# Kernel optimization log

Measured on AMD Instinct MI355X. Metric: run time of the kernel, lower is better.

The kernel has to match this reference:

```python
import jax, jax.numpy as jnp
import numpy as np

LN_EPS = 1e-12


def setup_inputs() -> dict:
    key = jax.random.key(0)
    ks = jax.random.split(key, 10)
    B, S, W, D, H = 16, 512, 5, 200, 768
    std = 0.02
    return {
        "layer_output": jax.random.normal(ks[0], (B, S, H), dtype=jnp.float32),
        "word_embeddings": jax.random.normal(ks[1], (B, S, W, D), dtype=jnp.float32),
        "word_mask": jax.random.randint(ks[2], (B, S, W), 0, 2, dtype=jnp.int64),
        "W1": jax.random.normal(ks[3], (D, H), dtype=jnp.float32) * std,
        "b1": jnp.zeros((H,), dtype=jnp.float32),
        "W2": jax.random.normal(ks[4], (H, H), dtype=jnp.float32) * std,
        "b2": jnp.zeros((H,), dtype=jnp.float32),
        "attn_W": jax.random.normal(ks[5], (H, H), dtype=jnp.float32) * std,
        "ln_gamma": jnp.ones((H,), dtype=jnp.float32),
        "ln_beta": jnp.zeros((H,), dtype=jnp.float32),
    }


def reference(layer_output, word_embeddings, word_mask, W1, b1, W2, b2, attn_W, ln_gamma, ln_beta):
    # word_transform: Linear -> Tanh -> Linear (dropout = identity in eval)
    we = jnp.tanh(jnp.einsum("bswd,dh->bswh", word_embeddings, W1) + b1)
    we = jnp.einsum("bswh,hk->bswk", we, W2) + b2  # [B,S,W,H]

    # bilinear word attention: (x @ attn_W) . word_outputs -> score over W
    q = jnp.einsum("bsh,hk->bsk", layer_output, attn_W)  # [B,S,H]
    alpha = jnp.einsum("bsk,bswk->bsw", q, we)            # [B,S,W]
    alpha = alpha + (1.0 - word_mask.astype(alpha.dtype)) * -10000.0
    alpha = jax.nn.softmax(alpha, axis=-1)

    # weighted sum over words + residual
    agg = jnp.einsum("bsw,bswh->bsh", alpha, we)
    h = layer_output + agg

    # LayerNorm (fuse_layer; dropout = identity in eval)
    mu = jnp.mean(h, axis=-1, keepdims=True)
    var = jnp.mean(jnp.square(h - mu), axis=-1, keepdims=True)
    return (h - mu) * jax.lax.rsqrt(var + LN_EPS) * ln_gamma + ln_beta
```

## Files before the change

kernel.cpp:

```cpp
#include <hip/hip_runtime.h>
#include <hip/hip_bf16.h>
#include <math.h>


typedef __attribute__((ext_vector_type(8))) short bf16x8;
typedef __attribute__((ext_vector_type(4))) float f32x4;

__device__ __forceinline__ unsigned short f2bf_bits(float f) {
    __hip_bfloat16 h = __float2bfloat16(f);
    return *reinterpret_cast<unsigned short*>(&h);
}
__device__ __forceinline__ float bf_bits2f(unsigned short u) {
    union { unsigned int i; float f; } v; v.i = ((unsigned int)u) << 16; return v.f;
}
__device__ __forceinline__ float tanh_fast(float x) {
    float xc = fminf(fmaxf(x, -9.f), 9.f);
    float t  = __expf(2.f * xc);
    return (t - 1.f) * __builtin_amdgcn_rcpf(t + 1.f);
}

__device__ __forceinline__ void async_cp16(const void* g, void* lds) {
#if __has_builtin(__builtin_amdgcn_global_load_lds)
    auto gp = (const __attribute__((address_space(1))) unsigned int*)g;
    auto lp = (__attribute__((address_space(3))) unsigned int*)lds;
    __builtin_amdgcn_global_load_lds(gp, lp, 16, 0, 0);
#else
    *(uint4*)lds = *(const uint4*)g;
#endif
}

template<bool HAS_BIAS, bool TANH_ACT, bool RESID, bool OUT_BF16, int N, int K, int GX>
__global__ __launch_bounds__(256) void mfma_gemm(
    const __hip_bfloat16* __restrict__ A,
    const __hip_bfloat16* __restrict__ Bt,
    const float* __restrict__ bias,
    const float* __restrict__ resid,
    void* __restrict__ outp)
{
    __shared__ __align__(16) unsigned char smem[32768];
    unsigned short* As = (unsigned short*)smem;
    unsigned short* Bs = (unsigned short*)(smem + 16384);

    int bx, by;
    {
        const int total = gridDim.x;
        const int per_xcd = total >> 3;
        if ((total & 7) == 0 && (per_xcd % GX) == 0) {
            int xcd = blockIdx.x & 7, idx = blockIdx.x >> 3;
            int lin = xcd * per_xcd + idx;
            by = lin / GX; bx = lin % GX;
        } else { by = blockIdx.x / GX; bx = blockIdx.x % GX; }
    }
    const int m0 = by * 128;
    const int n0 = bx * 128;

    const int tid  = threadIdx.x;
    const int lane = tid & 63;
    const int wave = tid >> 6;
    const int wm   = wave & 1;
    const int wn   = wave >> 1;

    const int rsub = lane >> 3;
    const int slot = lane & 7;
    const int kc   = slot ^ rsub;
    const __hip_bfloat16* gA = A  + (size_t)(m0 + wave * 32 + rsub) * K + kc * 8;
    const __hip_bfloat16* gB = Bt + (size_t)(n0 + wave * 32 + rsub) * K + kc * 8;
    unsigned short* lA = As + wave * 2048 + lane * 8;
    unsigned short* lB = Bs + wave * 2048 + lane * 8;

    const int row16 = lane & 15;
    const int kq    = lane >> 4;

    f32x4 acc[4][4];
#pragma unroll
    for (int i = 0; i < 4; i++)
#pragma unroll
        for (int j = 0; j < 4; j++) acc[i][j] = (f32x4){0.f, 0.f, 0.f, 0.f};

    for (int k0 = 0; k0 < K; k0 += 64) {
#pragma unroll
        for (int i = 0; i < 4; i++) {
            async_cp16(gA + i * 8 * K, lA + i * 512);
            async_cp16(gB + i * 8 * K, lB + i * 512);
        }
        gA += 64; gB += 64;
        __syncthreads();

        bf16x8 af[2][4], bg[2][4];
#pragma unroll
        for (int kh = 0; kh < 2; kh++) {
#pragma unroll
            for (int mi = 0; mi < 4; mi++) {
                const int r = wm * 64 + mi * 16 + row16;
                const int s = (kh * 4 + kq) ^ (r & 7);
                af[kh][mi] = *(const bf16x8*)&As[r * 64 + s * 8];
            }
#pragma unroll
            for (int ni = 0; ni < 4; ni++) {
                const int r = wn * 64 + ni * 16 + row16;
                const int s = (kh * 4 + kq) ^ (r & 7);
                bg[kh][ni] = *(const bf16x8*)&Bs[r * 64 + s * 8];
            }
        }
#pragma unroll
        for (int kh = 0; kh < 2; kh++)
#pragma unroll
            for (int mi = 0; mi < 4; mi++)
#pragma unroll
                for (int ni = 0; ni < 4; ni++)
                    acc[mi][ni] = __builtin_amdgcn_mfma_f32_16x16x32_bf16(
                        af[kh][mi], bg[kh][ni], acc[mi][ni], 0, 0, 0);
        __syncthreads();
    }

    if (OUT_BF16) {
        unsigned short* rep = (unsigned short*)smem;
#pragma unroll
        for (int ni = 0; ni < 4; ni++) {
            const int c = wn * 64 + ni * 16 + row16;
            float bcol = HAS_BIAS ? bias[n0 + c] : 0.f;
#pragma unroll
            for (int mi = 0; mi < 4; mi++)
#pragma unroll
                for (int r = 0; r < 4; r++) {
                    const int rr = wm * 64 + mi * 16 + kq * 4 + r;
                    float v = acc[mi][ni][r];
                    if (HAS_BIAS) v += bcol;
                    if (TANH_ACT) v = tanh_fast(v);
                    rep[rr * 128 + c] = f2bf_bits(v);
                }
        }
        __syncthreads();
#pragma unroll
        for (int p = 0; p < 8; p++) {
            const int lin = p * 256 + tid;
            const int row = lin >> 4;
            const int c8  = lin & 15;
            uint4 d = *(const uint4*)&rep[row * 128 + c8 * 8];
            *(uint4*)((__hip_bfloat16*)outp + (size_t)(m0 + row) * N + n0 + c8 * 8) = d;
        }
    } else {
        float* rep = (float*)smem;
#pragma unroll
        for (int h = 0; h < 2; h++) {
            if (wm == h) {
#pragma unroll
                for (int ni = 0; ni < 4; ni++) {
                    const int c = wn * 64 + ni * 16 + row16;
                    float bcol = HAS_BIAS ? bias[n0 + c] : 0.f;
#pragma unroll
                    for (int mi = 0; mi < 4; mi++)
#pragma unroll
                        for (int r = 0; r < 4; r++) {
                            const int rr = mi * 16 + kq * 4 + r;
                            float v = acc[mi][ni][r];
                            if (HAS_BIAS) v += bcol;
                            if (TANH_ACT) v = tanh_fast(v);
                            rep[rr * 128 + c] = v;
                        }
                }
            }
            __syncthreads();
#pragma unroll
            for (int p = 0; p < 8; p++) {
                const int lin = p * 256 + tid;
                const int row = lin >> 5;
                const int c4  = lin & 31;
                float4 v = *(const float4*)&rep[row * 128 + c4 * 4];
                const int grow = m0 + h * 64 + row;
                if (RESID) {
                    float4 rv = *(const float4*)&resid[(size_t)grow * N + n0 + c4 * 4];
                    v.x += rv.x; v.y += rv.y; v.z += rv.z; v.w += rv.w;
                }
                *(float4*)((float*)outp + (size_t)grow * N + n0 + c4 * 4) = v;
            }
            __syncthreads();
        }
    }
}

__global__ __launch_bounds__(256) void prep_kernel(
    const float* __restrict__ x,  __hip_bfloat16* __restrict__ xb,
    const float* __restrict__ w2, __hip_bfloat16* __restrict__ w2b,
    const float* __restrict__ aw, __hip_bfloat16* __restrict__ awb,
    const float* __restrict__ E,  __hip_bfloat16* __restrict__ Eb,
    const float* __restrict__ W1, __hip_bfloat16* __restrict__ W1Tb,
    __hip_bfloat16* __restrict__ W2Tb)
{
    __shared__ float tile[32][33];
    const int b = blockIdx.x, tid = threadIdx.x;
    if (b < 6144 + 576 + 576) {
        const float* src; __hip_bfloat16* dst; long long i;
        if (b < 6144)      { src = x;  dst = xb;  i = (long long)b * 256 + tid; }
        else if (b < 6720) { src = w2; dst = w2b; i = (long long)(b - 6144) * 256 + tid; }
        else               { src = aw; dst = awb; i = (long long)(b - 6720) * 256 + tid; }
        float4 v = ((const float4*)src)[i];
        ((ushort4*)dst)[i] = make_ushort4(f2bf_bits(v.x), f2bf_bits(v.y), f2bf_bits(v.z), f2bf_bits(v.w));
    } else if (b < 7296 + 10240) {
        const int lane = tid & 63, wave = tid >> 6;
        const long long row = (long long)(b - 7296) * 4 + wave;
        const int k = lane * 4;
        float4 v = make_float4(0.f, 0.f, 0.f, 0.f);
        if (k < 200) v = *(const float4*)&E[row * 200 + k];
        *(ushort4*)&Eb[row * 256 + k] =
            make_ushort4(f2bf_bits(v.x), f2bf_bits(v.y), f2bf_bits(v.z), f2bf_bits(v.w));
    } else {
        const float* in; __hip_bfloat16* outb; int R, C, Rpad, t;
        if (b < 17536 + 192) { t = b - 17536; in = W1; outb = W1Tb; R = 200; C = 768; Rpad = 256; }
        else                 { t = b - 17728; in = w2; outb = W2Tb; R = 768; C = 768; Rpad = 768; }
        const int c0 = (t % 24) * 32, r0 = (t / 24) * 32;
        const int xx = tid & 31, yy = tid >> 5;
#pragma unroll
        for (int i = 0; i < 32; i += 8) {
            int r = r0 + yy + i;
            tile[yy + i][xx] = (r < R) ? in[(size_t)r * C + c0 + xx] : 0.f;
        }
        __syncthreads();
#pragma unroll
        for (int i = 0; i < 32; i += 8)
            outb[(size_t)(c0 + yy + i) * Rpad + r0 + xx] = __float2bfloat16(tile[xx][yy + i]);
    }
}

__global__ __launch_bounds__(256) void attn_kernel(
    const __hip_bfloat16* __restrict__ T,
    const __hip_bfloat16* P,
    const int* __restrict__ mask,
    __hip_bfloat16* S)
{
    const int lane = threadIdx.x & 63;
    const int wave = threadIdx.x >> 6;
    const int r    = blockIdx.x * 4 + wave;
    const int base = lane * 12;

    float pv[12];
    {
        const ushort4* pp = (const ushort4*)((const unsigned short*)P + (size_t)r * 768 + base);
        ushort4 u0 = pp[0], u1 = pp[1], u2 = pp[2];
        unsigned short us[12] = {u0.x,u0.y,u0.z,u0.w, u1.x,u1.y,u1.z,u1.w, u2.x,u2.y,u2.z,u2.w};
#pragma unroll
        for (int j = 0; j < 12; j++) pv[j] = bf_bits2f(us[j]);
    }
    float tv[5][12], part[5];
#pragma unroll
    for (int w = 0; w < 5; w++) {
        const ushort4* tp = (const ushort4*)((const unsigned short*)T + ((size_t)r * 5 + w) * 768 + base);
        ushort4 u0 = tp[0], u1 = tp[1], u2 = tp[2];
        unsigned short us[12] = {u0.x,u0.y,u0.z,u0.w, u1.x,u1.y,u1.z,u1.w, u2.x,u2.y,u2.z,u2.w};
        float s = 0.f;
#pragma unroll
        for (int j = 0; j < 12; j++) { tv[w][j] = bf_bits2f(us[j]); s += tv[w][j] * pv[j]; }
        part[w] = s;
    }
#pragma unroll
    for (int off = 32; off > 0; off >>= 1)
#pragma unroll
        for (int w = 0; w < 5; w++)
            part[w] += __shfl_xor(part[w], off, 64);

    float logit[5], mx = -1e30f;
#pragma unroll
    for (int w = 0; w < 5; w++) {
        float m = (float)mask[(size_t)r * 5 + w];
        logit[w] = part[w] - 10000.0f * (1.0f - m);
        mx = fmaxf(mx, logit[w]);
    }
    float se = 0.f;
#pragma unroll
    for (int w = 0; w < 5; w++) { logit[w] = expf(logit[w] - mx); se += logit[w]; }
    const float inv = 1.0f / se;

    unsigned short os[12];
#pragma unroll
    for (int j = 0; j < 12; j++) {
        float s = 0.f;
#pragma unroll
        for (int w = 0; w < 5; w++) s += logit[w] * tv[w][j];
        os[j] = f2bf_bits(s * inv);
    }
    ushort4* sp = (ushort4*)((unsigned short*)S + (size_t)r * 768 + base);
    sp[0] = make_ushort4(os[0], os[1], os[2],  os[3]);
    sp[1] = make_ushort4(os[4], os[5], os[6],  os[7]);
    sp[2] = make_ushort4(os[8], os[9], os[10], os[11]);
}

__global__ __launch_bounds__(256) void ln_kernel(
    const float* __restrict__ Hbuf, const float* __restrict__ gamma,
    const float* __restrict__ beta, float* __restrict__ out)
{
    const int lane = threadIdx.x & 63;
    const int wave = threadIdx.x >> 6;
    const int r    = blockIdx.x * 4 + wave;
    const float* hr = Hbuf + (size_t)r * 768 + lane * 12;

    float v[12];
    {
        float4 a = *(const float4*)(hr);
        float4 b = *(const float4*)(hr + 4);
        float4 c = *(const float4*)(hr + 8);
        v[0]=a.x; v[1]=a.y; v[2]=a.z; v[3]=a.w;
        v[4]=b.x; v[5]=b.y; v[6]=b.z; v[7]=b.w;
        v[8]=c.x; v[9]=c.y; v[10]=c.z; v[11]=c.w;
    }
    float s = 0.f;
#pragma unroll
    for (int j = 0; j < 12; j++) s += v[j];
#pragma unroll
    for (int off = 32; off > 0; off >>= 1) s += __shfl_xor(s, off, 64);
    const float mu = s * (1.f / 768.f);
    float vs = 0.f;
#pragma unroll
    for (int j = 0; j < 12; j++) { float d = v[j] - mu; vs += d * d; }
#pragma unroll
    for (int off = 32; off > 0; off >>= 1) vs += __shfl_xor(vs, off, 64);
    const float rs = rsqrtf(vs * (1.f / 768.f) + 1e-12f);

    float o[12];
#pragma unroll
    for (int j = 0; j < 12; j++) {
        int h = lane * 12 + j;
        o[j] = (v[j] - mu) * rs * gamma[h] + beta[h];
    }
    float* orow = out + (size_t)r * 768 + lane * 12;
    *(float4*)(orow)     = make_float4(o[0], o[1], o[2],  o[3]);
    *(float4*)(orow + 4) = make_float4(o[4], o[5], o[6],  o[7]);
    *(float4*)(orow + 8) = make_float4(o[8], o[9], o[10], o[11]);
}

extern "C" void kernel_launch(void* const* d_in, const int* in_sizes, int n_in,
                              void* d_out, int out_size, void* d_ws, size_t ws_size,
                              hipStream_t stream)
{
    const float* x      = (const float*)d_in[0];
    const float* E      = (const float*)d_in[1];
    const int*   mask   = (const int*)d_in[2];
    const float* W1     = (const float*)d_in[3];
    const float* b1     = (const float*)d_in[4];
    const float* W2     = (const float*)d_in[5];
    const float* b2     = (const float*)d_in[6];
    const float* attn_W = (const float*)d_in[7];
    const float* gamma  = (const float*)d_in[8];
    const float* beta   = (const float*)d_in[9];
    float* out = (float*)d_out;

    const int BS = 8192, H = 768, M1 = 40960, KP = 256;

    char* p = (char*)d_ws;
    auto alloc = [&](size_t bytes) { char* q = p; p += (bytes + 255) & ~(size_t)255; return q; };
    __hip_bfloat16* xb    = (__hip_bfloat16*)alloc((size_t)BS * H * 2);
    __hip_bfloat16* W2b   = (__hip_bfloat16*)alloc((size_t)H * H * 2);
    __hip_bfloat16* W2Tb  = (__hip_bfloat16*)alloc((size_t)H * H * 2);
    __hip_bfloat16* attnb = (__hip_bfloat16*)alloc((size_t)H * H * 2);
    __hip_bfloat16* Ctb   = (__hip_bfloat16*)alloc((size_t)H * H * 2);
    __hip_bfloat16* W1Tb  = (__hip_bfloat16*)alloc((size_t)H * KP * 2);
    __hip_bfloat16* Tb    = (__hip_bfloat16*)alloc((size_t)M1 * H * 2);
    __hip_bfloat16* Eb    = (__hip_bfloat16*)alloc((size_t)M1 * KP * 2);
    float* Hb = (float*)Tb;
    __hip_bfloat16* Pb = Eb;
    __hip_bfloat16* Sb = Pb;

    prep_kernel<<<18304, 256, 0, stream>>>(x, xb, W2, W2b, attn_W, attnb,
                                           E, Eb, W1, W1Tb, W2Tb);

    mfma_gemm<false, false, false, true, 768, 768, 6><<<36, 256, 0, stream>>>(
        W2b, attnb, nullptr, nullptr, Ctb);
    mfma_gemm<true, true, false, true, 768, 256, 6><<<1920, 256, 0, stream>>>(
        Eb, W1Tb, b1, nullptr, Tb);
    mfma_gemm<false, false, false, true, 768, 768, 6><<<384, 256, 0, stream>>>(
        xb, Ctb, nullptr, nullptr, Pb);
    attn_kernel<<<BS / 4, 256, 0, stream>>>(Tb, Pb, mask, Sb);
    mfma_gemm<true, false, true, false, 768, 768, 6><<<384, 256, 0, stream>>>(
        Sb, W2Tb, b2, x, Hb);
    ln_kernel<<<BS / 4, 256, 0, stream>>>(Hb, gamma, beta, out);
}
```

Before: 234.0 us.

## Fuse fp32-to-bf16 conversion of inputs into GEMM tile loads

Removes the separate prep pass that converted x, W2, attn_W and the word embeddings to bf16 (with K padding to 256), and instead has the GEMM load fp32 directly, convert in registers and store bf16 into LDS, zero-masking K beyond 200. This avoids writing and re-reading large bf16 intermediate buffers, notably the 40960x256 embedding copy. The trade-off is that these loads become synchronous register loads instead of async global-to-LDS copies, which may reduce latency hiding inside the GEMM main loop.

```diff
diff --git a/kernel.cpp b/kernel.cpp
--- a/kernel.cpp
+++ b/kernel.cpp
@@ -29,10 +29,20 @@
 #endif
 }
 
-template<bool HAS_BIAS, bool TANH_ACT, bool RESID, bool OUT_BF16, int N, int K, int GX>
+__device__ __forceinline__ void cvt8_store(const float* src, bool valid, unsigned short* lds) {
+    float4 v0 = make_float4(0.f, 0.f, 0.f, 0.f), v1 = v0;
+    if (valid) { v0 = *(const float4*)src; v1 = *(const float4*)(src + 4); }
+    alignas(16) unsigned short h[8] = {
+        f2bf_bits(v0.x), f2bf_bits(v0.y), f2bf_bits(v0.z), f2bf_bits(v0.w),
+        f2bf_bits(v1.x), f2bf_bits(v1.y), f2bf_bits(v1.z), f2bf_bits(v1.w)};
+    *(uint4*)lds = *(const uint4*)h;
+}
+
+template<bool HAS_BIAS, bool TANH_ACT, bool RESID, bool OUT_BF16,
+         bool A_F32, bool B_F32, int N, int K, int KASRC, int GX>
 __global__ __launch_bounds__(256) void mfma_gemm(
-    const __hip_bfloat16* __restrict__ A,
-    const __hip_bfloat16* __restrict__ Bt,
+    const void* __restrict__ A,
+    const void* __restrict__ Bt,
     const float* __restrict__ bias,
     const float* __restrict__ resid,
     void* __restrict__ outp)
@@ -63,8 +73,11 @@
     const int rsub = lane >> 3;
     const int slot = lane & 7;
     const int kc   = slot ^ rsub;
-    const __hip_bfloat16* gA = A  + (size_t)(m0 + wave * 32 + rsub) * K + kc * 8;
-    const __hip_bfloat16* gB = Bt + (size_t)(n0 + wave * 32 + rsub) * K + kc * 8;
+
+    const __hip_bfloat16* gA = (const __hip_bfloat16*)A  + (size_t)(m0 + wave * 32 + rsub) * K + kc * 8;
+    const __hip_bfloat16* gB = (const __hip_bfloat16*)Bt + (size_t)(n0 + wave * 32 + rsub) * K + kc * 8;
+    const float* gAf = (const float*)A  + (size_t)(m0 + wave * 32 + rsub) * KASRC + kc * 8;
+    const float* gBf = (const float*)Bt + (size_t)(n0 + wave * 32 + rsub) * K + kc * 8;
     unsigned short* lA = As + wave * 2048 + lane * 8;
     unsigned short* lB = Bs + wave * 2048 + lane * 8;
 
@@ -78,12 +91,15 @@
         for (int j = 0; j < 4; j++) acc[i][j] = (f32x4){0.f, 0.f, 0.f, 0.f};
 
     for (int k0 = 0; k0 < K; k0 += 64) {
+        const bool avalid = !A_F32 || (k0 + kc * 8 < KASRC);
 #pragma unroll
         for (int i = 0; i < 4; i++) {
-            async_cp16(gA + i * 8 * K, lA + i * 512);
-            async_cp16(gB + i * 8 * K, lB + i * 512);
-        }
-        gA += 64; gB += 64;
+            if (A_F32) cvt8_store(gAf + (size_t)(8 * i) * KASRC, avalid, lA + i * 512);
+            else       async_cp16(gA + (size_t)(8 * i) * K, lA + i * 512);
+            if (B_F32) cvt8_store(gBf + (size_t)(8 * i) * K, true, lB + i * 512);
+            else       async_cp16(gB + (size_t)(8 * i) * K, lB + i * 512);
+        }
+        gA += 64; gB += 64; gAf += 64; gBf += 64;
         __syncthreads();
 
         bf16x8 af[2][4], bg[2][4];
@@ -180,46 +196,25 @@
 }
 
 __global__ __launch_bounds__(256) void prep_kernel(
-    const float* __restrict__ x,  __hip_bfloat16* __restrict__ xb,
-    const float* __restrict__ w2, __hip_bfloat16* __restrict__ w2b,
-    const float* __restrict__ aw, __hip_bfloat16* __restrict__ awb,
-    const float* __restrict__ E,  __hip_bfloat16* __restrict__ Eb,
     const float* __restrict__ W1, __hip_bfloat16* __restrict__ W1Tb,
-    __hip_bfloat16* __restrict__ W2Tb)
+    const float* __restrict__ W2, __hip_bfloat16* __restrict__ W2Tb)
 {
     __shared__ float tile[32][33];
     const int b = blockIdx.x, tid = threadIdx.x;
-    if (b < 6144 + 576 + 576) {
-        const float* src; __hip_bfloat16* dst; long long i;
-        if (b < 6144)      { src = x;  dst = xb;  i = (long long)b * 256 + tid; }
-        else if (b < 6720) { src = w2; dst = w2b; i = (long long)(b - 6144) * 256 + tid; }
-        else               { src = aw; dst = awb; i = (long long)(b - 6720) * 256 + tid; }
-        float4 v = ((const float4*)src)[i];
-        ((ushort4*)dst)[i] = make_ushort4(f2bf_bits(v.x), f2bf_bits(v.y), f2bf_bits(v.z), f2bf_bits(v.w));
-    } else if (b < 7296 + 10240) {
-        const int lane = tid & 63, wave = tid >> 6;
-        const long long row = (long long)(b - 7296) * 4 + wave;
-        const int k = lane * 4;
-        float4 v = make_float4(0.f, 0.f, 0.f, 0.f);
-        if (k < 200) v = *(const float4*)&E[row * 200 + k];
-        *(ushort4*)&Eb[row * 256 + k] =
-            make_ushort4(f2bf_bits(v.x), f2bf_bits(v.y), f2bf_bits(v.z), f2bf_bits(v.w));
-    } else {
-        const float* in; __hip_bfloat16* outb; int R, C, Rpad, t;
-        if (b < 17536 + 192) { t = b - 17536; in = W1; outb = W1Tb; R = 200; C = 768; Rpad = 256; }
-        else                 { t = b - 17728; in = w2; outb = W2Tb; R = 768; C = 768; Rpad = 768; }
-        const int c0 = (t % 24) * 32, r0 = (t / 24) * 32;
-        const int xx = tid & 31, yy = tid >> 5;
-#pragma unroll
-        for (int i = 0; i < 32; i += 8) {
-            int r = r0 + yy + i;
-            tile[yy + i][xx] = (r < R) ? in[(size_t)r * C + c0 + xx] : 0.f;
-        }
-        __syncthreads();
-#pragma unroll
-        for (int i = 0; i < 32; i += 8)
-            outb[(size_t)(c0 + yy + i) * Rpad + r0 + xx] = __float2bfloat16(tile[xx][yy + i]);
-    }
+    const float* in; __hip_bfloat16* outb; int R, C, Rpad, t;
+    if (b < 192) { t = b;       in = W1; outb = W1Tb; R = 200; C = 768; Rpad = 256; }
+    else         { t = b - 192; in = W2; outb = W2Tb; R = 768; C = 768; Rpad = 768; }
+    const int c0 = (t % 24) * 32, r0 = (t / 24) * 32;
+    const int xx = tid & 31, yy = tid >> 5;
+#pragma unroll
+    for (int i = 0; i < 32; i += 8) {
+        int r = r0 + yy + i;
+        tile[yy + i][xx] = (r < R) ? in[(size_t)r * C + c0 + xx] : 0.f;
+    }
+    __syncthreads();
+#pragma unroll
+    for (int i = 0; i < 32; i += 8)
+        outb[(size_t)(c0 + yy + i) * Rpad + r0 + xx] = __float2bfloat16(tile[xx][yy + i]);
 }
 
 __global__ __launch_bounds__(256) void attn_kernel(
@@ -347,29 +342,24 @@
 
     char* p = (char*)d_ws;
     auto alloc = [&](size_t bytes) { char* q = p; p += (bytes + 255) & ~(size_t)255; return q; };
-    __hip_bfloat16* xb    = (__hip_bfloat16*)alloc((size_t)BS * H * 2);
-    __hip_bfloat16* W2b   = (__hip_bfloat16*)alloc((size_t)H * H * 2);
     __hip_bfloat16* W2Tb  = (__hip_bfloat16*)alloc((size_t)H * H * 2);
-    __hip_bfloat16* attnb = (__hip_bfloat16*)alloc((size_t)H * H * 2);
     __hip_bfloat16* Ctb   = (__hip_bfloat16*)alloc((size_t)H * H * 2);
     __hip_bfloat16* W1Tb  = (__hip_bfloat16*)alloc((size_t)H * KP * 2);
     __hip_bfloat16* Tb    = (__hip_bfloat16*)alloc((size_t)M1 * H * 2);
-    __hip_bfloat16* Eb    = (__hip_bfloat16*)alloc((size_t)M1 * KP * 2);
+    __hip_bfloat16* Pb    = (__hip_bfloat16*)alloc((size_t)BS * H * 2);
     float* Hb = (float*)Tb;
-    __hip_bfloat16* Pb = Eb;
     __hip_bfloat16* Sb = Pb;
 
-    prep_kernel<<<18304, 256, 0, stream>>>(x, xb, W2, W2b, attn_W, attnb,
-                                           E, Eb, W1, W1Tb, W2Tb);
-
-    mfma_gemm<false, false, false, true, 768, 768, 6><<<36, 256, 0, stream>>>(
-        W2b, attnb, nullptr, nullptr, Ctb);
-    mfma_gemm<true, true, false, true, 768, 256, 6><<<1920, 256, 0, stream>>>(
-        Eb, W1Tb, b1, nullptr, Tb);
-    mfma_gemm<false, false, false, true, 768, 768, 6><<<384, 256, 0, stream>>>(
-        xb, Ctb, nullptr, nullptr, Pb);
+    prep_kernel<<<768, 256, 0, stream>>>(W1, W1Tb, W2, W2Tb);
+
+    mfma_gemm<false, false, false, true, true, true, 768, 768, 768, 6>
+        <<<36, 256, 0, stream>>>(W2, attn_W, nullptr, nullptr, Ctb);
+    mfma_gemm<true, true, false, true, true, false, 768, 256, 200, 6>
+        <<<1920, 256, 0, stream>>>(E, W1Tb, b1, nullptr, Tb);
+    mfma_gemm<false, false, false, true, true, false, 768, 768, 768, 6>
+        <<<384, 256, 0, stream>>>(x, Ctb, nullptr, nullptr, Pb);
     attn_kernel<<<BS / 4, 256, 0, stream>>>(Tb, Pb, mask, Sb);
-    mfma_gemm<true, false, true, false, 768, 768, 6><<<384, 256, 0, stream>>>(
-        Sb, W2Tb, b2, x, Hb);
+    mfma_gemm<true, false, true, false, false, false, 768, 768, 768, 6>
+        <<<384, 256, 0, stream>>>(Sb, W2Tb, b2, x, Hb);
     ln_kernel<<<BS / 4, 256, 0, stream>>>(Hb, gamma, beta, out);
 }
```

Result: slower. 251.4 us (+7.4%).

## Merge small Ct GEMM into first-layer GEMM launch and skip padded K tail

Applied to the files above, without the earlier changes.

Moves the GEMM body into a device function and launches the W2·attn_W product (36 tiles) and the E·W1 tanh GEMM (1920 tiles) together in one kernel. This removes a tiny, poorly occupied launch and the serialization between them. It also adds a KREAL template parameter so the padded last K half-step of the K=256 (real 200) GEMM skips its LDS reads and MFMAs. The K loop is now fully unrolled, which may raise register pressure or code size.

```diff
diff --git a/kernel.cpp b/kernel.cpp
--- a/kernel.cpp
+++ b/kernel.cpp
@@ -29,30 +29,17 @@
 #endif
 }
 
-template<bool HAS_BIAS, bool TANH_ACT, bool RESID, bool OUT_BF16, int N, int K, int GX>
-__global__ __launch_bounds__(256) void mfma_gemm(
+template<bool HAS_BIAS, bool TANH_ACT, bool RESID, bool OUT_BF16, int N, int K, int KREAL>
+__device__ __forceinline__ void gemm_body(
     const __hip_bfloat16* __restrict__ A,
     const __hip_bfloat16* __restrict__ Bt,
     const float* __restrict__ bias,
     const float* __restrict__ resid,
-    void* __restrict__ outp)
-{
-    __shared__ __align__(16) unsigned char smem[32768];
+    void* __restrict__ outp,
+    int m0, int n0, unsigned char* smem)
+{
     unsigned short* As = (unsigned short*)smem;
     unsigned short* Bs = (unsigned short*)(smem + 16384);
-
-    int bx, by;
-    {
-        const int total = gridDim.x;
-        const int per_xcd = total >> 3;
-        if ((total & 7) == 0 && (per_xcd % GX) == 0) {
-            int xcd = blockIdx.x & 7, idx = blockIdx.x >> 3;
-            int lin = xcd * per_xcd + idx;
-            by = lin / GX; bx = lin % GX;
-        } else { by = blockIdx.x / GX; bx = blockIdx.x % GX; }
-    }
-    const int m0 = by * 128;
-    const int n0 = bx * 128;
 
     const int tid  = threadIdx.x;
     const int lane = tid & 63;
@@ -77,39 +64,45 @@
 #pragma unroll
         for (int j = 0; j < 4; j++) acc[i][j] = (f32x4){0.f, 0.f, 0.f, 0.f};
 
+#pragma unroll
     for (int k0 = 0; k0 < K; k0 += 64) {
 #pragma unroll
         for (int i = 0; i < 4; i++) {
-            async_cp16(gA + i * 8 * K, lA + i * 512);
-            async_cp16(gB + i * 8 * K, lB + i * 512);
+            async_cp16(gA + (size_t)(8 * i) * K, lA + i * 512);
+            async_cp16(gB + (size_t)(8 * i) * K, lB + i * 512);
         }
         gA += 64; gB += 64;
         __syncthreads();
 
+        const bool full = (k0 + 32 < KREAL);
+
         bf16x8 af[2][4], bg[2][4];
 #pragma unroll
-        for (int kh = 0; kh < 2; kh++) {
-#pragma unroll
-            for (int mi = 0; mi < 4; mi++) {
-                const int r = wm * 64 + mi * 16 + row16;
-                const int s = (kh * 4 + kq) ^ (r & 7);
-                af[kh][mi] = *(const bf16x8*)&As[r * 64 + s * 8];
-            }
-#pragma unroll
-            for (int ni = 0; ni < 4; ni++) {
-                const int r = wn * 64 + ni * 16 + row16;
-                const int s = (kh * 4 + kq) ^ (r & 7);
-                bg[kh][ni] = *(const bf16x8*)&Bs[r * 64 + s * 8];
-            }
-        }
-#pragma unroll
-        for (int kh = 0; kh < 2; kh++)
+        for (int mi = 0; mi < 4; mi++) {
+            const int r = wm * 64 + mi * 16 + row16;
+            af[0][mi] = *(const bf16x8*)&As[r * 64 + (kq ^ (r & 7)) * 8];
+            if (full) af[1][mi] = *(const bf16x8*)&As[r * 64 + ((4 + kq) ^ (r & 7)) * 8];
+        }
+#pragma unroll
+        for (int ni = 0; ni < 4; ni++) {
+            const int r = wn * 64 + ni * 16 + row16;
+            bg[0][ni] = *(const bf16x8*)&Bs[r * 64 + (kq ^ (r & 7)) * 8];
+            if (full) bg[1][ni] = *(const bf16x8*)&Bs[r * 64 + ((4 + kq) ^ (r & 7)) * 8];
+        }
+#pragma unroll
+        for (int mi = 0; mi < 4; mi++)
+#pragma unroll
+            for (int ni = 0; ni < 4; ni++)
+                acc[mi][ni] = __builtin_amdgcn_mfma_f32_16x16x32_bf16(
+                    af[0][mi], bg[0][ni], acc[mi][ni], 0, 0, 0);
+        if (full) {
 #pragma unroll
             for (int mi = 0; mi < 4; mi++)
 #pragma unroll
                 for (int ni = 0; ni < 4; ni++)
                     acc[mi][ni] = __builtin_amdgcn_mfma_f32_16x16x32_bf16(
-                        af[kh][mi], bg[kh][ni], acc[mi][ni], 0, 0, 0);
+                        af[1][mi], bg[1][ni], acc[mi][ni], 0, 0, 0);
+        }
         __syncthreads();
     }
 
@@ -176,6 +169,48 @@
             }
             __syncthreads();
         }
+    }
+}
+
+template<bool HAS_BIAS, bool TANH_ACT, bool RESID, bool OUT_BF16, int N, int K, int GX>
+__global__ __launch_bounds__(256) void mfma_gemm(
+    const __hip_bfloat16* __restrict__ A,
+    const __hip_bfloat16* __restrict__ Bt,
+    const float* __restrict__ bias,
+    const float* __restrict__ resid,
+    void* __restrict__ outp)
+{
+    __shared__ __align__(16) unsigned char smem[32768];
+    int bx, by;
+    {
+        const int total = gridDim.x;
+        const int per_xcd = total >> 3;
+        if ((total & 7) == 0 && (per_xcd % GX) == 0) {
+            int xcd = blockIdx.x & 7, idx = blockIdx.x >> 3;
+            int lin = xcd * per_xcd + idx;
+            by = lin / GX; bx = lin % GX;
+        } else { by = blockIdx.x / GX; bx = blockIdx.x % GX; }
+    }
+    gemm_body<HAS_BIAS, TANH_ACT, RESID, OUT_BF16, N, K, K>(
+        A, Bt, bias, resid, outp, by * 128, bx * 128, smem);
+}
+
+__global__ __launch_bounds__(256) void tct_kernel(
+    const __hip_bfloat16* __restrict__ Eb,   const __hip_bfloat16* __restrict__ W1Tb,
+    const float* __restrict__ b1,            __hip_bfloat16* __restrict__ Tb,
+    const __hip_bfloat16* __restrict__ W2b,  const __hip_bfloat16* __restrict__ attnb,
+    __hip_bfloat16* __restrict__ Ctb)
+{
+    __shared__ __align__(16) unsigned char smem[32768];
+    if (blockIdx.x < 1920) {
+        const int xcd = blockIdx.x & 7, idx = blockIdx.x >> 3;
+        const int lin = xcd * 240 + idx;
+        gemm_body<true, true, false, true, 768, 256, 224>(
+            Eb, W1Tb, b1, nullptr, Tb, (lin / 6) * 128, (lin % 6) * 128, smem);
+    } else {
+        const int id = blockIdx.x - 1920;
+        gemm_body<false, false, false, true, 768, 768, 768>(
+            W2b, attnb, nullptr, nullptr, Ctb, (id / 6) * 128, (id % 6) * 128, smem);
     }
 }
 
@@ -362,10 +397,8 @@
     prep_kernel<<<18304, 256, 0, stream>>>(x, xb, W2, W2b, attn_W, attnb,
                                            E, Eb, W1, W1Tb, W2Tb);
 
-    mfma_gemm<false, false, false, true, 768, 768, 6><<<36, 256, 0, stream>>>(
-        W2b, attnb, nullptr, nullptr, Ctb);
-    mfma_gemm<true, true, false, true, 768, 256, 6><<<1920, 256, 0, stream>>>(
-        Eb, W1Tb, b1, nullptr, Tb);
+    tct_kernel<<<1956, 256, 0, stream>>>(Eb, W1Tb, b1, Tb, W2b, attnb, Ctb);
+
     mfma_gemm<false, false, false, true, 768, 768, 6><<<384, 256, 0, stream>>>(
         xb, Ctb, nullptr, nullptr, Pb);
     attn_kernel<<<BS / 4, 256, 0, stream>>>(Tb, Pb, mask, Sb);
```

Result: faster. 216.5 us (-7.5%).
